# Kernel tuning notes

Measured on AMD Instinct MI355X. Metric: run time of the kernel, lower is better.

The kernel has to match this reference:

```python
import jax, jax.numpy as jnp
import numpy as np

ATT_TIMES = 2
EPS = 1e-12  # torch F.normalize eps

N_NODES = 200000
EMB_DIM = 256
ATT_NUM = 2


def setup_inputs() -> dict:
    key = jax.random.key(0)
    k1, k2 = jax.random.split(key)
    x = jax.random.normal(k1, (N_NODES, EMB_DIM), dtype=jnp.float32)
    # glorot/xavier-normal init for the att_num projection matrices W_i
    std = float(np.sqrt(2.0 / (EMB_DIM + EMB_DIM)))
    W = jax.random.normal(k2, (ATT_NUM, EMB_DIM, EMB_DIM), dtype=jnp.float32) * std
    return {"x": x, "W": W}


def _one_attention(x, Wi):
    """One attention head (att_style='dot', att_weight=True), iterated ATT_TIMES."""
    xi = x
    out = None
    for _ in range(ATT_TIMES):
        temp = jnp.mean(xi, axis=0, keepdims=True)          # (1, D)
        h_avg = jnp.tanh(temp @ Wi)                          # (1, D)
        # 'dot' style: interact with W = identity -> scores = x @ h_avg^T, (N, 1)
        scores = xi @ h_avg.T                                # (N, 1)
        # F.normalize(p=1, dim=1) on an (N,1) column: divide by max(|v|, eps)
        norm = jnp.maximum(jnp.sum(jnp.abs(scores), axis=1, keepdims=True), EPS)
        att = jax.nn.sigmoid(scores / norm)                  # (N, 1)
        out = att.T @ xi                                     # (1, D)
        xi = xi * att                                        # re-weight for next round
    return out


def reference(x, W):
    att_num = W.shape[0]
    outs = [_one_attention(x, W[i]) for i in range(att_num)]
    return jnp.concatenate(outs, axis=1)                     # (1, att_num * D)
```

## Files before the change

### kernel.cpp

```cpp
#include <hip/hip_runtime.h>
#include <math.h>

#define NROWS 200000
#define D 256
#define F4 64

#define NBLK 1250
#define CHUNK 160
#define ITERS 10

#define WS_H1 0
#define WS_H2 512
#define WS_A  1024
#define WS_P1 401024
#define WS_P2 721024

__device__ __forceinline__ float att_sigmoid(float s) {
    float t = s / fmaxf(fabsf(s), 1e-12f);
    return 1.0f / (1.0f + __expf(-t));
}

__device__ __forceinline__ float dot4(float4 a, float4 b) {
    return fmaf(a.x, b.x, fmaf(a.y, b.y, fmaf(a.z, b.z, a.w * b.w)));
}

__device__ __forceinline__ float group16_sum(float v) {
#pragma unroll
    for (int off = 1; off < 16; off <<= 1) v += __shfl_xor(v, off);
    return v;
}

__global__ void __launch_bounds__(256) colsum_kernel(const float* __restrict__ x,
                                                     float* __restrict__ part) {
    const int tid = threadIdx.x, lane = tid & 63, wv = tid >> 6;
    const float4* x4 = reinterpret_cast<const float4*>(x);
    const size_t base = (size_t)(blockIdx.x * CHUNK + wv * 4) * F4 + lane;
    float4 cur[4], nxt[4];
#pragma unroll
    for (int j = 0; j < 4; ++j) cur[j] = x4[base + j * F4];
    float4 accA = make_float4(0.f, 0.f, 0.f, 0.f);
    float4 accB = make_float4(0.f, 0.f, 0.f, 0.f);
    for (int it = 0; it < ITERS; ++it) {
        if (it + 1 < ITERS) {
            size_t nb = base + (size_t)(it + 1) * 16 * F4;
#pragma unroll
            for (int j = 0; j < 4; ++j) nxt[j] = x4[nb + j * F4];
        }
        accA.x += cur[0].x + cur[1].x; accB.x += cur[2].x + cur[3].x;
        accA.y += cur[0].y + cur[1].y; accB.y += cur[2].y + cur[3].y;
        accA.z += cur[0].z + cur[1].z; accB.z += cur[2].z + cur[3].z;
        accA.w += cur[0].w + cur[1].w; accB.w += cur[2].w + cur[3].w;
        if (it + 1 < ITERS) {
#pragma unroll
            for (int j = 0; j < 4; ++j) cur[j] = nxt[j];
        }
    }
    accA.x += accB.x; accA.y += accB.y; accA.z += accB.z; accA.w += accB.w;
    __shared__ float4 sh[256];
    sh[tid] = accA;
    __syncthreads();
    if (tid < 64) {
        float4 a = sh[tid], b = sh[tid + 64], c = sh[tid + 128], d = sh[tid + 192];
        float4 s;
        s.x = (a.x + b.x) + (c.x + d.x);
        s.y = (a.y + b.y) + (c.y + d.y);
        s.z = (a.z + b.z) + (c.z + d.z);
        s.w = (a.w + b.w) + (c.w + d.w);
        reinterpret_cast<float4*>(part)[blockIdx.x * 64 + tid] = s;
    }
}

__global__ void __launch_bounds__(256) hproj_fused(const float* __restrict__ W,
                                                   const float* __restrict__ part,
                                                   int width4, int headOff4, float scale,
                                                   float* __restrict__ hout) {
    const int head = blockIdx.x;
    const int tid = threadIdx.x, lane = tid & 63, wv = tid >> 6;
    const float4* p4 = reinterpret_cast<const float4*>(part) + head * headOff4 + lane;
    float4 s = make_float4(0.f, 0.f, 0.f, 0.f);
#pragma unroll 5
    for (int r = wv; r < NBLK; r += 4) {
        float4 v = p4[(size_t)r * width4];
        s.x += v.x; s.y += v.y; s.z += v.z; s.w += v.w;
    }
    __shared__ float4 red[4][64];
    __shared__ float vbuf[D];
    red[wv][lane] = s;
    __syncthreads();
    if (tid < 64) {
        float4 a = red[0][tid], b = red[1][tid], c = red[2][tid], d = red[3][tid];
        vbuf[tid * 4 + 0] = ((a.x + b.x) + (c.x + d.x)) * scale;
        vbuf[tid * 4 + 1] = ((a.y + b.y) + (c.y + d.y)) * scale;
        vbuf[tid * 4 + 2] = ((a.z + b.z) + (c.z + d.z)) * scale;
        vbuf[tid * 4 + 3] = ((a.w + b.w) + (c.w + d.w)) * scale;
    }
    __syncthreads();
    const float* Wh = W + head * D * D;
    float acc = 0.0f;
#pragma unroll 8
    for (int k = 0; k < D; ++k) acc = fmaf(vbuf[k], Wh[k * D + tid], acc);
    hout[head * D + tid] = tanhf(acc);
}

__global__ void __launch_bounds__(256) pass1_kernel(const float* __restrict__ x,
                                                    float* __restrict__ ws) {
    const float* h = ws + WS_H1;
    float* aA0 = ws + WS_A;
    float* aA1 = ws + WS_A + NROWS;
    float* part = ws + WS_P2;
    const int tid = threadIdx.x, lane = tid & 63, wv = tid >> 6;
    const int sub = lane >> 4, li = lane & 15;
    const float4* x4 = reinterpret_cast<const float4*>(x);
    const float4* h4 = reinterpret_cast<const float4*>(h);
    float4 h0v[4], h1v[4];
#pragma unroll
    for (int t = 0; t < 4; ++t) { h0v[t] = h4[li + 16 * t]; h1v[t] = h4[64 + li + 16 * t]; }
    const int row0 = blockIdx.x * CHUNK + wv * 4 + sub;
    const size_t base = (size_t)row0 * F4 + li;
    float4 cur[4], nxt[4];
#pragma unroll
    for (int t = 0; t < 4; ++t) cur[t] = x4[base + 16 * t];
    float4 acc0[4], acc1[4];
#pragma unroll
    for (int t = 0; t < 4; ++t) {
        acc0[t] = make_float4(0.f, 0.f, 0.f, 0.f);
        acc1[t] = make_float4(0.f, 0.f, 0.f, 0.f);
    }
    for (int it = 0; it < ITERS; ++it) {
        if (it + 1 < ITERS) {
            size_t nb = base + (size_t)(it + 1) * 16 * F4;
#pragma unroll
            for (int t = 0; t < 4; ++t) nxt[t] = x4[nb + 16 * t];
        }
        float d0 = (dot4(cur[0], h0v[0]) + dot4(cur[1], h0v[1]))
                 + (dot4(cur[2], h0v[2]) + dot4(cur[3], h0v[3]));
        float d1 = (dot4(cur[0], h1v[0]) + dot4(cur[1], h1v[1]))
                 + (dot4(cur[2], h1v[2]) + dot4(cur[3], h1v[3]));
        d0 = group16_sum(d0);
        d1 = group16_sum(d1);
        float a0 = att_sigmoid(d0);
        float a1 = att_sigmoid(d1);
        if (li == 0) {
            aA0[row0 + it * 16] = a0;
            aA1[row0 + it * 16] = a1;
        }
#pragma unroll
        for (int t = 0; t < 4; ++t) {
            acc0[t].x = fmaf(a0, cur[t].x, acc0[t].x);
            acc0[t].y = fmaf(a0, cur[t].y, acc0[t].y);
            acc0[t].z = fmaf(a0, cur[t].z, acc0[t].z);
            acc0[t].w = fmaf(a0, cur[t].w, acc0[t].w);
            acc1[t].x = fmaf(a1, cur[t].x, acc1[t].x);
            acc1[t].y = fmaf(a1, cur[t].y, acc1[t].y);
            acc1[t].z = fmaf(a1, cur[t].z, acc1[t].z);
            acc1[t].w = fmaf(a1, cur[t].w, acc1[t].w);
        }
        if (it + 1 < ITERS) {
#pragma unroll
            for (int t = 0; t < 4; ++t) cur[t] = nxt[t];
        }
    }
    __shared__ float4 sh[256][9];
#pragma unroll
    for (int t = 0; t < 4; ++t) { sh[tid][t] = acc0[t]; sh[tid][4 + t] = acc1[t]; }
    __syncthreads();
    if (tid < 128) {
        const int hh = tid >> 6, f = tid & 63, fl = f & 15, ft = f >> 4;
        float4 s = make_float4(0.f, 0.f, 0.f, 0.f);
#pragma unroll
        for (int g = 0; g < 16; ++g) {
            float4 v = sh[(g >> 2) * 64 + (g & 3) * 16 + fl][hh * 4 + ft];
            s.x += v.x; s.y += v.y; s.z += v.z; s.w += v.w;
        }
        reinterpret_cast<float4*>(part)[blockIdx.x * 128 + tid] = s;
    }
}

__global__ void __launch_bounds__(256) pass2_kernel(const float* __restrict__ x,
                                                    float* __restrict__ ws) {
    const float* h = ws + WS_H2;
    const float* aA0 = ws + WS_A;
    const float* aA1 = ws + WS_A + NROWS;
    float* part = ws + WS_P2;
    const int tid = threadIdx.x, lane = tid & 63, wv = tid >> 6;
    const int sub = lane >> 4, li = lane & 15;
    const float4* x4 = reinterpret_cast<const float4*>(x);
    const float4* h4 = reinterpret_cast<const float4*>(h);
    float4 h0v[4], h1v[4];
#pragma unroll
    for (int t = 0; t < 4; ++t) { h0v[t] = h4[li + 16 * t]; h1v[t] = h4[64 + li + 16 * t]; }
    const int row0 = blockIdx.x * CHUNK + wv * 4 + sub;
    const size_t base = (size_t)row0 * F4 + li;
    float4 cur[4], nxt[4];
    float caa0, caa1, naa0, naa1;
#pragma unroll
    for (int t = 0; t < 4; ++t) cur[t] = x4[base + 16 * t];
    caa0 = aA0[row0];
    caa1 = aA1[row0];
    float4 acc0[4], acc1[4];
#pragma unroll
    for (int t = 0; t < 4; ++t) {
        acc0[t] = make_float4(0.f, 0.f, 0.f, 0.f);
        acc1[t] = make_float4(0.f, 0.f, 0.f, 0.f);
    }
    for (int it = 0; it < ITERS; ++it) {
        if (it + 1 < ITERS) {
            size_t nb = base + (size_t)(it + 1) * 16 * F4;
#pragma unroll
            for (int t = 0; t < 4; ++t) nxt[t] = x4[nb + 16 * t];
            naa0 = aA0[row0 + (it + 1) * 16];
            naa1 = aA1[row0 + (it + 1) * 16];
        }
        float d0 = (dot4(cur[0], h0v[0]) + dot4(cur[1], h0v[1]))
                 + (dot4(cur[2], h0v[2]) + dot4(cur[3], h0v[3]));
        float d1 = (dot4(cur[0], h1v[0]) + dot4(cur[1], h1v[1]))
                 + (dot4(cur[2], h1v[2]) + dot4(cur[3], h1v[3]));
        d0 = group16_sum(d0);
        d1 = group16_sum(d1);
        float w0 = att_sigmoid(caa0 * d0) * caa0;
        float w1 = att_sigmoid(caa1 * d1) * caa1;
#pragma unroll
        for (int t = 0; t < 4; ++t) {
            acc0[t].x = fmaf(w0, cur[t].x, acc0[t].x);
            acc0[t].y = fmaf(w0, cur[t].y, acc0[t].y);
            acc0[t].z = fmaf(w0, cur[t].z, acc0[t].z);
            acc0[t].w = fmaf(w0, cur[t].w, acc0[t].w);
            acc1[t].x = fmaf(w1, cur[t].x, acc1[t].x);
            acc1[t].y = fmaf(w1, cur[t].y, acc1[t].y);
            acc1[t].z = fmaf(w1, cur[t].z, acc1[t].z);
            acc1[t].w = fmaf(w1, cur[t].w, acc1[t].w);
        }
        if (it + 1 < ITERS) {
#pragma unroll
            for (int t = 0; t < 4; ++t) cur[t] = nxt[t];
            caa0 = naa0; caa1 = naa1;
        }
    }
    __shared__ float4 sh[256][9];
#pragma unroll
    for (int t = 0; t < 4; ++t) { sh[tid][t] = acc0[t]; sh[tid][4 + t] = acc1[t]; }
    __syncthreads();
    if (tid < 128) {
        const int hh = tid >> 6, f = tid & 63, fl = f & 15, ft = f >> 4;
        float4 s = make_float4(0.f, 0.f, 0.f, 0.f);
#pragma unroll
        for (int g = 0; g < 16; ++g) {
            float4 v = sh[(g >> 2) * 64 + (g & 3) * 16 + fl][hh * 4 + ft];
            s.x += v.x; s.y += v.y; s.z += v.z; s.w += v.w;
        }
        reinterpret_cast<float4*>(part)[blockIdx.x * 128 + tid] = s;
    }
}

__global__ void __launch_bounds__(256) out_reduce(const float* __restrict__ part,
                                                  float* __restrict__ out) {
    const int head = blockIdx.x;
    const int tid = threadIdx.x, lane = tid & 63, wv = tid >> 6;
    const float4* p4 = reinterpret_cast<const float4*>(part) + head * 64 + lane;
    float4 s = make_float4(0.f, 0.f, 0.f, 0.f);
#pragma unroll 5
    for (int r = wv; r < NBLK; r += 4) {
        float4 v = p4[(size_t)r * 128];
        s.x += v.x; s.y += v.y; s.z += v.z; s.w += v.w;
    }
    __shared__ float4 red[4][64];
    red[wv][lane] = s;
    __syncthreads();
    if (tid < 64) {
        float4 a = red[0][tid], b = red[1][tid], c = red[2][tid], d = red[3][tid];
        float4 o;
        o.x = (a.x + b.x) + (c.x + d.x);
        o.y = (a.y + b.y) + (c.y + d.y);
        o.z = (a.z + b.z) + (c.z + d.z);
        o.w = (a.w + b.w) + (c.w + d.w);
        reinterpret_cast<float4*>(out)[head * 64 + tid] = o;
    }
}

extern "C" void kernel_launch(void* const* d_in, const int* in_sizes, int n_in,
                              void* d_out, int out_size, void* d_ws, size_t ws_size,
                              hipStream_t stream) {
    const float* x = (const float*)d_in[0];
    const float* W = (const float*)d_in[1];
    float* out = (float*)d_out;
    float* ws = (float*)d_ws;

    colsum_kernel<<<dim3(NBLK), dim3(256), 0, stream>>>(x, ws + WS_P1);
    hproj_fused<<<dim3(2), dim3(256), 0, stream>>>(W, ws + WS_P1, 64, 0, 1.0f / NROWS, ws + WS_H1);
    pass1_kernel<<<dim3(NBLK), dim3(256), 0, stream>>>(x, ws);
    hproj_fused<<<dim3(2), dim3(256), 0, stream>>>(W, ws + WS_P2, 128, 64, 1.0f / NROWS, ws + WS_H2);
    pass2_kernel<<<dim3(NBLK), dim3(256), 0, stream>>>(x, ws);
    out_reduce<<<dim3(2), dim3(256), 0, stream>>>(ws + WS_P2, out);
}
```

Before: 184.3 us.

## Cast x to bf16 copy in colsum pass and fuse tail reductions via last-block atomics

```diff
diff --git a/kernel.cpp b/kernel.cpp
--- a/kernel.cpp
+++ b/kernel.cpp
@@ -5,43 +5,54 @@
 #define D 256
 #define F4 64
 
-#define NBLK 1250
-#define CHUNK 160
-#define ITERS 10
+#define NBLK 500
+#define CHUNK 400
+#define CITERS 25
+#define PITERS 10
 
 #define WS_H1 0
 #define WS_H2 512
-#define WS_A  1024
-#define WS_P1 401024
-#define WS_P2 721024
+#define WS_TK 1024
+#define WS_A  1040
+#define WS_P1 401040
+#define WS_P2 529040
+#define WS_XB 785040
 
 __device__ __forceinline__ float att_sigmoid(float s) {
     float t = s / fmaxf(fabsf(s), 1e-12f);
     return 1.0f / (1.0f + __expf(-t));
 }
 
-__device__ __forceinline__ float dot4(float4 a, float4 b) {
-    return fmaf(a.x, b.x, fmaf(a.y, b.y, fmaf(a.z, b.z, a.w * b.w)));
-}
-
-__device__ __forceinline__ float group16_sum(float v) {
-#pragma unroll
-    for (int off = 1; off < 16; off <<= 1) v += __shfl_xor(v, off);
-    return v;
-}
-
-__global__ void __launch_bounds__(256) colsum_kernel(const float* __restrict__ x,
-                                                     float* __restrict__ part) {
+__device__ __forceinline__ unsigned int packbf2(float a, float b) {
+    unsigned int ua = __float_as_uint(a);
+    unsigned int ub = __float_as_uint(b);
+    ua = (ua + 0x7FFFu + ((ua >> 16) & 1u)) >> 16;
+    ub = (ub + 0x7FFFu + ((ub >> 16) & 1u)) >> 16;
+    return ua | (ub << 16);
+}
+
+__device__ __forceinline__ void unpack8(uint4 q, float* f) {
+    f[0] = __uint_as_float(q.x << 16); f[1] = __uint_as_float(q.x & 0xFFFF0000u);
+    f[2] = __uint_as_float(q.y << 16); f[3] = __uint_as_float(q.y & 0xFFFF0000u);
+    f[4] = __uint_as_float(q.z << 16); f[5] = __uint_as_float(q.z & 0xFFFF0000u);
+    f[6] = __uint_as_float(q.w << 16); f[7] = __uint_as_float(q.w & 0xFFFF0000u);
+}
+
+__global__ void __launch_bounds__(256) colsum_cast_h1(const float* __restrict__ x,
+                                                      const float* __restrict__ W,
+                                                      float* __restrict__ ws,
+                                                      uint2* __restrict__ xb2) {
     const int tid = threadIdx.x, lane = tid & 63, wv = tid >> 6;
     const float4* x4 = reinterpret_cast<const float4*>(x);
-    const size_t base = (size_t)(blockIdx.x * CHUNK + wv * 4) * F4 + lane;
+    const int r0 = blockIdx.x * CHUNK + wv * 4;
+    const size_t base = (size_t)r0 * F4 + lane;
     float4 cur[4], nxt[4];
 #pragma unroll
     for (int j = 0; j < 4; ++j) cur[j] = x4[base + j * F4];
     float4 accA = make_float4(0.f, 0.f, 0.f, 0.f);
     float4 accB = make_float4(0.f, 0.f, 0.f, 0.f);
-    for (int it = 0; it < ITERS; ++it) {
-        if (it + 1 < ITERS) {
+    for (int it = 0; it < CITERS; ++it) {
+        if (it + 1 < CITERS) {
             size_t nb = base + (size_t)(it + 1) * 16 * F4;
 #pragma unroll
             for (int j = 0; j < 4; ++j) nxt[j] = x4[nb + j * F4];
@@ -50,7 +61,13 @@
         accA.y += cur[0].y + cur[1].y; accB.y += cur[2].y + cur[3].y;
         accA.z += cur[0].z + cur[1].z; accB.z += cur[2].z + cur[3].z;
         accA.w += cur[0].w + cur[1].w; accB.w += cur[2].w + cur[3].w;
-        if (it + 1 < ITERS) {
+        const int rb = r0 + it * 16;
+#pragma unroll
+        for (int j = 0; j < 4; ++j) {
+            xb2[(size_t)(rb + j) * 64 + lane] =
+                make_uint2(packbf2(cur[j].x, cur[j].y), packbf2(cur[j].z, cur[j].w));
+        }
+        if (it + 1 < CITERS) {
 #pragma unroll
             for (int j = 0; j < 4; ++j) cur[j] = nxt[j];
         }
@@ -66,214 +83,268 @@
         s.y = (a.y + b.y) + (c.y + d.y);
         s.z = (a.z + b.z) + (c.z + d.z);
         s.w = (a.w + b.w) + (c.w + d.w);
-        reinterpret_cast<float4*>(part)[blockIdx.x * 64 + tid] = s;
-    }
-}
-
-__global__ void __launch_bounds__(256) hproj_fused(const float* __restrict__ W,
-                                                   const float* __restrict__ part,
-                                                   int width4, int headOff4, float scale,
-                                                   float* __restrict__ hout) {
-    const int head = blockIdx.x;
-    const int tid = threadIdx.x, lane = tid & 63, wv = tid >> 6;
-    const float4* p4 = reinterpret_cast<const float4*>(part) + head * headOff4 + lane;
-    float4 s = make_float4(0.f, 0.f, 0.f, 0.f);
+        reinterpret_cast<float4*>(ws + WS_P1)[blockIdx.x * 64 + tid] = s;
+    }
+    __threadfence();
+    __shared__ unsigned win;
+    if (tid == 0) {
+        unsigned old = atomicAdd(reinterpret_cast<unsigned*>(ws + WS_TK) + 0, 1u);
+        win = (old == NBLK - 1) ? 1u : 0u;
+    }
+    __syncthreads();
+    if (win) {
+        __threadfence();
+        const float4* p14 = reinterpret_cast<const float4*>(ws + WS_P1);
+        const int c4 = tid & 63, rg = tid >> 6;
+        float4 s = make_float4(0.f, 0.f, 0.f, 0.f);
 #pragma unroll 5
-    for (int r = wv; r < NBLK; r += 4) {
-        float4 v = p4[(size_t)r * width4];
-        s.x += v.x; s.y += v.y; s.z += v.z; s.w += v.w;
-    }
-    __shared__ float4 red[4][64];
-    __shared__ float vbuf[D];
-    red[wv][lane] = s;
-    __syncthreads();
-    if (tid < 64) {
-        float4 a = red[0][tid], b = red[1][tid], c = red[2][tid], d = red[3][tid];
-        vbuf[tid * 4 + 0] = ((a.x + b.x) + (c.x + d.x)) * scale;
-        vbuf[tid * 4 + 1] = ((a.y + b.y) + (c.y + d.y)) * scale;
-        vbuf[tid * 4 + 2] = ((a.z + b.z) + (c.z + d.z)) * scale;
-        vbuf[tid * 4 + 3] = ((a.w + b.w) + (c.w + d.w)) * scale;
-    }
-    __syncthreads();
-    const float* Wh = W + head * D * D;
-    float acc = 0.0f;
+        for (int r = rg; r < NBLK; r += 4) {
+            float4 v = p14[r * 64 + c4];
+            s.x += v.x; s.y += v.y; s.z += v.z; s.w += v.w;
+        }
+        __syncthreads();
+        sh[tid] = s;
+        __syncthreads();
+        __shared__ float vb[D];
+        if (tid < 64) {
+            float4 a = sh[tid], b = sh[tid + 64], c = sh[tid + 128], d = sh[tid + 192];
+            const float sc = 1.0f / NROWS;
+            vb[tid * 4 + 0] = ((a.x + b.x) + (c.x + d.x)) * sc;
+            vb[tid * 4 + 1] = ((a.y + b.y) + (c.y + d.y)) * sc;
+            vb[tid * 4 + 2] = ((a.z + b.z) + (c.z + d.z)) * sc;
+            vb[tid * 4 + 3] = ((a.w + b.w) + (c.w + d.w)) * sc;
+        }
+        __syncthreads();
+        float a0 = 0.f, a1 = 0.f;
 #pragma unroll 8
-    for (int k = 0; k < D; ++k) acc = fmaf(vbuf[k], Wh[k * D + tid], acc);
-    hout[head * D + tid] = tanhf(acc);
-}
-
-__global__ void __launch_bounds__(256) pass1_kernel(const float* __restrict__ x,
-                                                    float* __restrict__ ws) {
-    const float* h = ws + WS_H1;
+        for (int k = 0; k < D; ++k) {
+            float vk = vb[k];
+            a0 = fmaf(vk, W[k * D + tid], a0);
+            a1 = fmaf(vk, W[D * D + k * D + tid], a1);
+        }
+        ws[WS_H1 + tid] = tanhf(a0);
+        ws[WS_H1 + D + tid] = tanhf(a1);
+    }
+}
+
+__global__ void __launch_bounds__(256) pass1_b(const uint4* __restrict__ xb,
+                                               const float* __restrict__ W,
+                                               float* __restrict__ ws) {
     float* aA0 = ws + WS_A;
     float* aA1 = ws + WS_A + NROWS;
     float* part = ws + WS_P2;
+    const float* h = ws + WS_H1;
     const int tid = threadIdx.x, lane = tid & 63, wv = tid >> 6;
-    const int sub = lane >> 4, li = lane & 15;
-    const float4* x4 = reinterpret_cast<const float4*>(x);
-    const float4* h4 = reinterpret_cast<const float4*>(h);
-    float4 h0v[4], h1v[4];
-#pragma unroll
-    for (int t = 0; t < 4; ++t) { h0v[t] = h4[li + 16 * t]; h1v[t] = h4[64 + li + 16 * t]; }
-    const int row0 = blockIdx.x * CHUNK + wv * 4 + sub;
-    const size_t base = (size_t)row0 * F4 + li;
-    float4 cur[4], nxt[4];
-#pragma unroll
-    for (int t = 0; t < 4; ++t) cur[t] = x4[base + 16 * t];
-    float4 acc0[4], acc1[4];
-#pragma unroll
-    for (int t = 0; t < 4; ++t) {
-        acc0[t] = make_float4(0.f, 0.f, 0.f, 0.f);
-        acc1[t] = make_float4(0.f, 0.f, 0.f, 0.f);
-    }
-    for (int it = 0; it < ITERS; ++it) {
-        if (it + 1 < ITERS) {
-            size_t nb = base + (size_t)(it + 1) * 16 * F4;
-#pragma unroll
-            for (int t = 0; t < 4; ++t) nxt[t] = x4[nb + 16 * t];
-        }
-        float d0 = (dot4(cur[0], h0v[0]) + dot4(cur[1], h0v[1]))
-                 + (dot4(cur[2], h0v[2]) + dot4(cur[3], h0v[3]));
-        float d1 = (dot4(cur[0], h1v[0]) + dot4(cur[1], h1v[1]))
-                 + (dot4(cur[2], h1v[2]) + dot4(cur[3], h1v[3]));
-        d0 = group16_sum(d0);
-        d1 = group16_sum(d1);
-        float a0 = att_sigmoid(d0);
-        float a1 = att_sigmoid(d1);
-        if (li == 0) {
-            aA0[row0 + it * 16] = a0;
-            aA1[row0 + it * 16] = a1;
-        }
-#pragma unroll
-        for (int t = 0; t < 4; ++t) {
-            acc0[t].x = fmaf(a0, cur[t].x, acc0[t].x);
-            acc0[t].y = fmaf(a0, cur[t].y, acc0[t].y);
-            acc0[t].z = fmaf(a0, cur[t].z, acc0[t].z);
-            acc0[t].w = fmaf(a0, cur[t].w, acc0[t].w);
-            acc1[t].x = fmaf(a1, cur[t].x, acc1[t].x);
-            acc1[t].y = fmaf(a1, cur[t].y, acc1[t].y);
-            acc1[t].z = fmaf(a1, cur[t].z, acc1[t].z);
-            acc1[t].w = fmaf(a1, cur[t].w, acc1[t].w);
-        }
-        if (it + 1 < ITERS) {
-#pragma unroll
-            for (int t = 0; t < 4; ++t) cur[t] = nxt[t];
-        }
-    }
-    __shared__ float4 sh[256][9];
-#pragma unroll
-    for (int t = 0; t < 4; ++t) { sh[tid][t] = acc0[t]; sh[tid][4 + t] = acc1[t]; }
-    __syncthreads();
-    if (tid < 128) {
-        const int hh = tid >> 6, f = tid & 63, fl = f & 15, ft = f >> 4;
+    const int hi = lane >> 5, chunk = lane & 31, c0 = chunk * 8;
+    const int w0 = blockIdx.x * CHUNK + wv * 100;
+    float hh0[8], hh1[8];
+#pragma unroll
+    for (int k = 0; k < 8; ++k) { hh0[k] = h[c0 + k]; hh1[k] = h[D + c0 + k]; }
+    float acc0[8], acc1[8];
+#pragma unroll
+    for (int k = 0; k < 8; ++k) { acc0[k] = 0.f; acc1[k] = 0.f; }
+    const size_t base = (size_t)w0 * 32;
+    uint4 cur[5], nxt[5];
+#pragma unroll
+    for (int q = 0; q < 5; ++q) cur[q] = xb[base + q * 64 + lane];
+    for (int it = 0; it < PITERS; ++it) {
+        if (it + 1 < PITERS) {
+            const size_t nb = base + (size_t)(it + 1) * 320;
+#pragma unroll
+            for (int q = 0; q < 5; ++q) nxt[q] = xb[nb + q * 64 + lane];
+        }
+        float d0[5], d1[5];
+#pragma unroll
+        for (int q = 0; q < 5; ++q) {
+            float f[8];
+            unpack8(cur[q], f);
+            float s0 = 0.f, s1 = 0.f;
+#pragma unroll
+            for (int k = 0; k < 8; ++k) { s0 = fmaf(f[k], hh0[k], s0); s1 = fmaf(f[k], hh1[k], s1); }
+            d0[q] = s0; d1[q] = s1;
+        }
+#pragma unroll
+        for (int q = 0; q < 5; ++q) {
+#pragma unroll
+            for (int off = 1; off < 32; off <<= 1) {
+                d0[q] += __shfl_xor(d0[q], off);
+                d1[q] += __shfl_xor(d1[q], off);
+            }
+        }
+        const int rb = w0 + it * 10;
+#pragma unroll
+        for (int q = 0; q < 5; ++q) {
+            float a0 = att_sigmoid(d0[q]);
+            float a1 = att_sigmoid(d1[q]);
+            if (chunk == 0) { aA0[rb + 2 * q + hi] = a0; aA1[rb + 2 * q + hi] = a1; }
+            float f[8];
+            unpack8(cur[q], f);
+#pragma unroll
+            for (int k = 0; k < 8; ++k) {
+                acc0[k] = fmaf(a0, f[k], acc0[k]);
+                acc1[k] = fmaf(a1, f[k], acc1[k]);
+            }
+        }
+#pragma unroll
+        for (int q = 0; q < 5; ++q) cur[q] = nxt[q];
+    }
+    __shared__ float lds[256][17];
+#pragma unroll
+    for (int k = 0; k < 8; ++k) { lds[tid][k] = acc0[k]; lds[tid][8 + k] = acc1[k]; }
+    __syncthreads();
+    {
+        float s0 = 0.f, s1 = 0.f;
+#pragma unroll
+        for (int g = 0; g < 8; ++g) {
+            s0 += lds[g * 32 + (tid >> 3)][tid & 7];
+            s1 += lds[g * 32 + (tid >> 3)][8 + (tid & 7)];
+        }
+        part[blockIdx.x * 512 + tid] = s0;
+        part[blockIdx.x * 512 + 256 + tid] = s1;
+    }
+    __threadfence();
+    __shared__ unsigned win;
+    if (tid == 0) {
+        unsigned old = atomicAdd(reinterpret_cast<unsigned*>(ws + WS_TK) + 1, 1u);
+        win = (old == NBLK - 1) ? 1u : 0u;
+    }
+    __syncthreads();
+    if (win) {
+        __threadfence();
+        const float4* p4 = reinterpret_cast<const float4*>(ws + WS_P2);
+        const int c4 = tid & 127, rg = tid >> 7;
         float4 s = make_float4(0.f, 0.f, 0.f, 0.f);
-#pragma unroll
-        for (int g = 0; g < 16; ++g) {
-            float4 v = sh[(g >> 2) * 64 + (g & 3) * 16 + fl][hh * 4 + ft];
+#pragma unroll 5
+        for (int r = rg; r < NBLK; r += 2) {
+            float4 v = p4[r * 128 + c4];
             s.x += v.x; s.y += v.y; s.z += v.z; s.w += v.w;
         }
-        reinterpret_cast<float4*>(part)[blockIdx.x * 128 + tid] = s;
-    }
-}
-
-__global__ void __launch_bounds__(256) pass2_kernel(const float* __restrict__ x,
-                                                    float* __restrict__ ws) {
-    const float* h = ws + WS_H2;
+        __shared__ float4 red[256];
+        red[tid] = s;
+        __syncthreads();
+        __shared__ float vb[2 * D];
+        if (tid < 128) {
+            float4 a = red[tid], b = red[128 + tid];
+            const float sc = 1.0f / NROWS;
+            vb[tid * 4 + 0] = (a.x + b.x) * sc;
+            vb[tid * 4 + 1] = (a.y + b.y) * sc;
+            vb[tid * 4 + 2] = (a.z + b.z) * sc;
+            vb[tid * 4 + 3] = (a.w + b.w) * sc;
+        }
+        __syncthreads();
+        float a0 = 0.f, a1 = 0.f;
+#pragma unroll 8
+        for (int k = 0; k < D; ++k) {
+            a0 = fmaf(vb[k], W[k * D + tid], a0);
+            a1 = fmaf(vb[D + k], W[D * D + k * D + tid], a1);
+        }
+        ws[WS_H2 + tid] = tanhf(a0);
+        ws[WS_H2 + D + tid] = tanhf(a1);
+    }
+}
+
+__global__ void __launch_bounds__(256) pass2_b(const uint4* __restrict__ xb,
+                                               float* __restrict__ ws,
+                                               float* __restrict__ out) {
     const float* aA0 = ws + WS_A;
     const float* aA1 = ws + WS_A + NROWS;
     float* part = ws + WS_P2;
+    const float* h = ws + WS_H2;
     const int tid = threadIdx.x, lane = tid & 63, wv = tid >> 6;
-    const int sub = lane >> 4, li = lane & 15;
-    const float4* x4 = reinterpret_cast<const float4*>(x);
-    const float4* h4 = reinterpret_cast<const float4*>(h);
-    float4 h0v[4], h1v[4];
-#pragma unroll
-    for (int t = 0; t < 4; ++t) { h0v[t] = h4[li + 16 * t]; h1v[t] = h4[64 + li + 16 * t]; }
-    const int row0 = blockIdx.x * CHUNK + wv * 4 + sub;
-    const size_t base = (size_t)row0 * F4 + li;
-    float4 cur[4], nxt[4];
-    float caa0, caa1, naa0, naa1;
-#pragma unroll
-    for (int t = 0; t < 4; ++t) cur[t] = x4[base + 16 * t];
-    caa0 = aA0[row0];
-    caa1 = aA1[row0];
-    float4 acc0[4], acc1[4];
-#pragma unroll
-    for (int t = 0; t < 4; ++t) {
-        acc0[t] = make_float4(0.f, 0.f, 0.f, 0.f);
-        acc1[t] = make_float4(0.f, 0.f, 0.f, 0.f);
-    }
-    for (int it = 0; it < ITERS; ++it) {
-        if (it + 1 < ITERS) {
-            size_t nb = base + (size_t)(it + 1) * 16 * F4;
-#pragma unroll
-            for (int t = 0; t < 4; ++t) nxt[t] = x4[nb + 16 * t];
-            naa0 = aA0[row0 + (it + 1) * 16];
-            naa1 = aA1[row0 + (it + 1) * 16];
-        }
-        float d0 = (dot4(cur[0], h0v[0]) + dot4(cur[1], h0v[1]))
-                 + (dot4(cur[2], h0v[2]) + dot4(cur[3], h0v[3]));
-        float d1 = (dot4(cur[0], h1v[0]) + dot4(cur[1], h1v[1]))
-                 + (dot4(cur[2], h1v[2]) + dot4(cur[3], h1v[3]));
-        d0 = group16_sum(d0);
-        d1 = group16_sum(d1);
-        float w0 = att_sigmoid(caa0 * d0) * caa0;
-        float w1 = att_sigmoid(caa1 * d1) * caa1;
-#pragma unroll
-        for (int t = 0; t < 4; ++t) {
-            acc0[t].x = fmaf(w0, cur[t].x, acc0[t].x);
-            acc0[t].y = fmaf(w0, cur[t].y, acc0[t].y);
-            acc0[t].z = fmaf(w0, cur[t].z, acc0[t].z);
-            acc0[t].w = fmaf(w0, cur[t].w, acc0[t].w);
-            acc1[t].x = fmaf(w1, cur[t].x, acc1[t].x);
-            acc1[t].y = fmaf(w1, cur[t].y, acc1[t].y);
-            acc1[t].z = fmaf(w1, cur[t].z, acc1[t].z);
-            acc1[t].w = fmaf(w1, cur[t].w, acc1[t].w);
-        }
-        if (it + 1 < ITERS) {
-#pragma unroll
-            for (int t = 0; t < 4; ++t) cur[t] = nxt[t];
-            caa0 = naa0; caa1 = naa1;
-        }
-    }
-    __shared__ float4 sh[256][9];
-#pragma unroll
-    for (int t = 0; t < 4; ++t) { sh[tid][t] = acc0[t]; sh[tid][4 + t] = acc1[t]; }
-    __syncthreads();
-    if (tid < 128) {
-        const int hh = tid >> 6, f = tid & 63, fl = f & 15, ft = f >> 4;
+    const int hi = lane >> 5, chunk = lane & 31, c0 = chunk * 8;
+    const int w0 = blockIdx.x * CHUNK + wv * 100;
+    float hh0[8], hh1[8];
+#pragma unroll
+    for (int k = 0; k < 8; ++k) { hh0[k] = h[c0 + k]; hh1[k] = h[D + c0 + k]; }
+    float acc0[8], acc1[8];
+#pragma unroll
+    for (int k = 0; k < 8; ++k) { acc0[k] = 0.f; acc1[k] = 0.f; }
+    const size_t base = (size_t)w0 * 32;
+    uint4 cur[5], nxt[5];
+#pragma unroll
+    for (int q = 0; q < 5; ++q) cur[q] = xb[base + q * 64 + lane];
+    for (int it = 0; it < PITERS; ++it) {
+        if (it + 1 < PITERS) {
+            const size_t nb = base + (size_t)(it + 1) * 320;
+#pragma unroll
+            for (int q = 0; q < 5; ++q) nxt[q] = xb[nb + q * 64 + lane];
+        }
+        float d0[5], d1[5];
+#pragma unroll
+        for (int q = 0; q < 5; ++q) {
+            float f[8];
+            unpack8(cur[q], f);
+            float s0 = 0.f, s1 = 0.f;
+#pragma unroll
+            for (int k = 0; k < 8; ++k) { s0 = fmaf(f[k], hh0[k], s0); s1 = fmaf(f[k], hh1[k], s1); }
+            d0[q] = s0; d1[q] = s1;
+        }
+#pragma unroll
+        for (int q = 0; q < 5; ++q) {
+#pragma unroll
+            for (int off = 1; off < 32; off <<= 1) {
+                d0[q] += __shfl_xor(d0[q], off);
+                d1[q] += __shfl_xor(d1[q], off);
+            }
+        }
+        const int rb = w0 + it * 10;
+#pragma unroll
+        for (int q = 0; q < 5; ++q) {
+            float aa0 = aA0[rb + 2 * q + hi];
+            float aa1 = aA1[rb + 2 * q + hi];
+            float w0h = att_sigmoid(aa0 * d0[q]) * aa0;
+            float w1h = att_sigmoid(aa1 * d1[q]) * aa1;
+            float f[8];
+            unpack8(cur[q], f);
+#pragma unroll
+            for (int k = 0; k < 8; ++k) {
+                acc0[k] = fmaf(w0h, f[k], acc0[k]);
+                acc1[k] = fmaf(w1h, f[k], acc1[k]);
+            }
+        }
+#pragma unroll
+        for (int q = 0; q < 5; ++q) cur[q] = nxt[q];
+    }
+    __shared__ float lds[256][17];
+#pragma unroll
+    for (int k = 0; k < 8; ++k) { lds[tid][k] = acc0[k]; lds[tid][8 + k] = acc1[k]; }
+    __syncthreads();
+    {
+        float s0 = 0.f, s1 = 0.f;
+#pragma unroll
+        for (int g = 0; g < 8; ++g) {
+            s0 += lds[g * 32 + (tid >> 3)][tid & 7];
+            s1 += lds[g * 32 + (tid >> 3)][8 + (tid & 7)];
+        }
+        part[blockIdx.x * 512 + tid] = s0;
+        part[blockIdx.x * 512 + 256 + tid] = s1;
+    }
+    __threadfence();
+    __shared__ unsigned win;
+    if (tid == 0) {
+        unsigned old = atomicAdd(reinterpret_cast<unsigned*>(ws + WS_TK) + 2, 1u);
+        win = (old == NBLK - 1) ? 1u : 0u;
+    }
+    __syncthreads();
+    if (win) {
+        __threadfence();
+        const float4* p4 = reinterpret_cast<const float4*>(ws + WS_P2);
+        const int c4 = tid & 127, rg = tid >> 7;
         float4 s = make_float4(0.f, 0.f, 0.f, 0.f);
-#pragma unroll
-        for (int g = 0; g < 16; ++g) {
-            float4 v = sh[(g >> 2) * 64 + (g & 3) * 16 + fl][hh * 4 + ft];
+#pragma unroll 5
+        for (int r = rg; r < NBLK; r += 2) {
+            float4 v = p4[r * 128 + c4];
             s.x += v.x; s.y += v.y; s.z += v.z; s.w += v.w;
         }
-        reinterpret_cast<float4*>(part)[blockIdx.x * 128 + tid] = s;
-    }
-}
-
-__global__ void __launch_bounds__(256) out_reduce(const float* __restrict__ part,
-                                                  float* __restrict__ out) {
-    const int head = blockIdx.x;
-    const int tid = threadIdx.x, lane = tid & 63, wv = tid >> 6;
-    const float4* p4 = reinterpret_cast<const float4*>(part) + head * 64 + lane;
-    float4 s = make_float4(0.f, 0.f, 0.f, 0.f);
-#pragma unroll 5
-    for (int r = wv; r < NBLK; r += 4) {
-        float4 v = p4[(size_t)r * 128];
-        s.x += v.x; s.y += v.y; s.z += v.z; s.w += v.w;
-    }
-    __shared__ float4 red[4][64];
-    red[wv][lane] = s;
-    __syncthreads();
-    if (tid < 64) {
-        float4 a = red[0][tid], b = red[1][tid], c = red[2][tid], d = red[3][tid];
-        float4 o;
-        o.x = (a.x + b.x) + (c.x + d.x);
-        o.y = (a.y + b.y) + (c.y + d.y);
-        o.z = (a.z + b.z) + (c.z + d.z);
-        o.w = (a.w + b.w) + (c.w + d.w);
-        reinterpret_cast<float4*>(out)[head * 64 + tid] = o;
+        __shared__ float4 red[256];
+        red[tid] = s;
+        __syncthreads();
+        if (tid < 128) {
+            float4 a = red[tid], b = red[128 + tid];
+            float4 o;
+            o.x = a.x + b.x; o.y = a.y + b.y; o.z = a.z + b.z; o.w = a.w + b.w;
+            reinterpret_cast<float4*>(out)[tid] = o;
+        }
     }
 }
 
@@ -285,10 +356,11 @@
     float* out = (float*)d_out;
     float* ws = (float*)d_ws;
 
-    colsum_kernel<<<dim3(NBLK), dim3(256), 0, stream>>>(x, ws + WS_P1);
-    hproj_fused<<<dim3(2), dim3(256), 0, stream>>>(W, ws + WS_P1, 64, 0, 1.0f / NROWS, ws + WS_H1);
-    pass1_kernel<<<dim3(NBLK), dim3(256), 0, stream>>>(x, ws);
-    hproj_fused<<<dim3(2), dim3(256), 0, stream>>>(W, ws + WS_P2, 128, 64, 1.0f / NROWS, ws + WS_H2);
-    pass2_kernel<<<dim3(NBLK), dim3(256), 0, stream>>>(x, ws);
-    out_reduce<<<dim3(2), dim3(256), 0, stream>>>(ws + WS_P2, out);
-}
+    uint2* xb2 = reinterpret_cast<uint2*>(ws + WS_XB);
+    const uint4* xb4 = reinterpret_cast<const uint4*>(ws + WS_XB);
+
+    hipMemsetAsync(ws + WS_TK, 0, 64, stream);
+    colsum_cast_h1<<<dim3(NBLK), dim3(256), 0, stream>>>(x, W, ws, xb2);
+    pass1_b<<<dim3(NBLK), dim3(256), 0, stream>>>(xb4, W, ws);
+    pass2_b<<<dim3(NBLK), dim3(256), 0, stream>>>(xb4, ws, out);
+}
```

Result: slower. 342.3 us (+85.8%).
